# Optimization experiments

Measured on AMD Instinct MI355X. Metric: run time of the kernel, lower is better.

The kernel has to match this reference:

```python
import jax, jax.numpy as jnp
import numpy as np

# dims
V = 50000      # vocab_size
DW = 50        # word_embed_size
DP = 5         # pos_embed_size
D = DW + 2 * DP  # input_size = 60
OC = 230       # out_c
NREL = 53      # n_rel
POSV = 61      # 2*pos_limit + 1
LIMIT = 30     # piecewise split threshold
G, B, L = 1000, 8, 120  # n_bags, bag_size, sentence length


def setup_inputs() -> dict:
    key = jax.random.key(0)
    ks = jax.random.split(key, 11)
    f32 = jnp.float32
    words = jax.random.randint(ks[0], (G, B, L), 0, V, dtype=jnp.int32)
    pos = jax.random.randint(ks[1], (G, B, L, 2), 0, POSV, dtype=jnp.int32)
    # pretrained-style word embeddings + position embeddings
    w2v = jax.random.normal(ks[2], (V, DW), f32) * 0.1
    pos1_emb = jax.random.normal(ks[3], (POSV, DP), f32) * 0.1
    pos2_emb = jax.random.normal(ks[4], (POSV, DP), f32) * 0.1
    con1 = float(np.sqrt(6.0 / ((DP + DW) * 3)))
    conv_w = jax.random.uniform(ks[5], (OC, 1, 3, D), f32, -con1, con1)  # OIHW
    conv_b0 = jax.random.uniform(ks[6], (1, OC), f32, -con1, con1)
    conv_b1 = jax.random.uniform(ks[7], (1, OC), f32, -con1, con1)
    conv_b2 = jax.random.uniform(ks[8], (1, OC), f32, -con1, con1)
    con = float(np.sqrt(6.0 / (OC + NREL)))
    r_embed = jax.random.uniform(ks[9], (NREL, 3 * OC), f32, -con, con)
    r_bias = jax.random.uniform(ks[10], (NREL,), f32, -con, con)
    return dict(words=words, pos=pos, w2v=w2v, pos1_emb=pos1_emb,
                pos2_emb=pos2_emb, conv_w=conv_w, conv_b0=conv_b0,
                conv_b1=conv_b1, conv_b2=conv_b2, r_embed=r_embed,
                r_bias=r_bias)


def reference(words, pos, w2v, pos1_emb, pos2_emb, conv_w,
              conv_b0, conv_b1, conv_b2, r_embed, r_bias):
    g, bag, ln = words.shape
    n = g * bag
    w = words.reshape(n, ln)
    p = pos.reshape(n, ln, 2)
    # embedding lookups -> [N, L, D]
    x = jnp.concatenate([w2v[w], pos1_emb[p[..., 0]], pos2_emb[p[..., 1]]], axis=-1)
    # Conv1d(1, OC, (3, D), padding=(1, 0)) over [N,1,L,D] -> [N,OC,L]
    feat = jax.lax.conv_general_dilated(
        x[:, None, :, :], conv_w, window_strides=(1, 1),
        padding=((1, 1), (0, 0)),
        dimension_numbers=('NCHW', 'OIHW', 'NCHW'))[..., 0]
    # piecewise masks from position ids
    p1 = (p[..., 0] >= LIMIT).astype(feat.dtype)  # [N, L]
    p2 = (p[..., 1] >= LIMIT).astype(feat.dtype)
    left = p1 * p2
    right = (1.0 - p1) * (1.0 - p2)
    mid = 1.0 - left - right

    def pool(mask, bias):  # masked max over sequence + per-piece bias
        return jnp.max(feat * mask[:, None, :], axis=-1) + bias  # [N, OC]

    f = jnp.concatenate([pool(left, conv_b0), pool(mid, conv_b1),
                         pool(right, conv_b2)], axis=-1)  # [N, 3*OC]
    f = jnp.tanh(f)
    # eval mode: dropout identity, logits scaled by 0.5 before bias
    logits = (f @ r_embed.T) * 0.5 + r_bias  # [N, NREL]
    logp = jax.nn.log_softmax(logits, axis=-1).reshape(g, bag, NREL)
    # eval mode: max over sentences in each bag
    return jnp.max(logp, axis=1)  # [G, NREL]
```

## Files before the change

kernel.cpp:

```cpp
#include <hip/hip_runtime.h>
#include <hip/hip_bf16.h>
#include <math.h>

typedef __bf16 bf16;
typedef __bf16 bf16x4 __attribute__((ext_vector_type(4)));
typedef __bf16 bf16x8 __attribute__((ext_vector_type(8)));
typedef float f32x4 __attribute__((ext_vector_type(4)));

#define OCC 230
#define NRELS 53
#define PCAT_OFF 2500000
#define REMBB_OFF 2537216
#define CONVB_OFF 2582272
#define ZOFF 2631424
#define WS_ELEMS 2631432

union FragU { bf16x8 v8; bf16x4 v4[2]; bf16 e[8]; };

__global__ void pcnn_prep(const float* __restrict__ w2v, const float* __restrict__ p1e,
                          const float* __restrict__ p2e, const float* __restrict__ remb,
                          const float* __restrict__ convw, bf16* __restrict__ wsb) {
  const int i = blockIdx.x * 256 + threadIdx.x;
  if (i < 625000) {
    const float4 f = *reinterpret_cast<const float4*>(w2v + 4 * i);
    bf16x4 v = {(bf16)f.x, (bf16)f.y, (bf16)f.z, (bf16)f.w};
    *reinterpret_cast<bf16x4*>(wsb + 4 * i) = v;
    return;
  }
  int e = i - 625000;
  if (e < 37210) {
    const int row = e / 10, c = e - row * 10;
    const int v1 = row / 61, v2 = row - v1 * 61;
    wsb[PCAT_OFF + e] = (bf16)((c < 5) ? p1e[v1 * 5 + c] : p2e[v2 * 5 + (c - 5)]);
    return;
  }
  e -= 37210;
  if (e < 45056) {
    const int r = e / 704, c = e - r * 704;
    wsb[REMBB_OFF + e] = (r < NRELS && c < 690) ? (bf16)remb[r * 690 + c] : (bf16)0.0f;
    return;
  }
  e -= 45056;
  if (e < 49152) {
    const int oc = e / 192, k = e - oc * 192;
    wsb[CONVB_OFF + e] = (oc < OCC && k < 180) ? (bf16)convw[oc * 180 + k] : (bf16)0.0f;
    return;
  }
  e -= 49152;
  if (e < 8) wsb[ZOFF + e] = (bf16)0.0f;
}

__global__ __launch_bounds__(1024, 4)
void pcnn_bag(const int* __restrict__ words, const int* __restrict__ posi,
              const float* __restrict__ cb0, const float* __restrict__ cb1,
              const float* __restrict__ cb2, const float* __restrict__ rbias,
              const bf16* __restrict__ wsb, float* __restrict__ out)
{
  __shared__ __align__(16) bf16 xflat[2][7360];
  __shared__ __align__(16) bf16 fl_all[8][712];
  __shared__ int widx[960];
  __shared__ float poolbuf[2][3][256];
  __shared__ float logits_l[8][64];

  const int t = threadIdx.x;
  const int b = blockIdx.x;
  const int wv = t >> 6;
  const int lane = t & 63;
  const int g = lane >> 4;
  const int cl = lane & 15;
  const int mh = wv >> 3;
  const int ocp = wv & 7;

  if (t < 960) {
    const int w = words[b * 960 + t];
    const int2 pp = *reinterpret_cast<const int2*>(posi + b * 1920 + 2 * t);
    const bool b0 = pp.x >= 30, b1 = pp.y >= 30;
    const int pc = (b0 && b1) ? 0 : ((!b0 && !b1) ? 2 : 1);
    widx[t] = w | ((pp.x * 61 + pp.y) << 16) | (pc << 28);
  }
  if (t < 60) { xflat[0][t] = (bf16)0.0f; xflat[1][t] = (bf16)0.0f; }
  if (t < 112) fl_all[t / 14][690 + (t % 14)] = (bf16)0.0f;

  FragU Bf[2][6];
  {
    const bf16* cwb = wsb + CONVB_OFF;
#pragma unroll
    for (int nt = 0; nt < 2; ++nt) {
      const int oc = ocp * 32 + nt * 16 + cl;
#pragma unroll
      for (int ks = 0; ks < 6; ++ks)
        Bf[nt][ks].v8 = *reinterpret_cast<const bf16x8*>(cwb + oc * 192 + ks * 32 + g * 8);
    }
  }

  int pA = 0, ocA = 0;
  float biasA = 0.0f;
  if (t < 690) {
    pA = t / 230; ocA = t - pA * 230;
    biasA = (pA == 0 ? cb0 : pA == 1 ? cb1 : cb2)[ocA];
  }
  __syncthreads();

  auto gather_one = [&](int s, int nb, int j) {
    const int q = j * 1024 + wv * 64 + lane;
    const int qc = (q < 3600) ? q : 3599;
    const int l = qc / 30;
    const int c = qc - l * 30;
    const int wi = widx[s * 120 + l];
    const int word = wi & 0xFFFF;
    const int pidx = (wi >> 16) & 0xFFF;
    const bf16* srcd = (c < 25) ? (wsb + word * 50 + 2 * c)
                                : (wsb + PCAT_OFF + pidx * 10 + (2 * c - 50));
    const bf16* src = (q < 3600) ? srcd : (wsb + ZOFF);
    bf16* dst = &xflat[nb][60 + j * 2048 + wv * 128];
    __builtin_amdgcn_global_load_lds(
        (const __attribute__((address_space(1))) void*)src,
        (__attribute__((address_space(3))) void*)dst, 4, 0, 0);
  };
  auto issue_gather = [&](int s, int nb) {
#pragma unroll
    for (int j = 0; j < 3; ++j) gather_one(s, nb, j);
    if (wv < 9) gather_one(s, nb, 3);
  };

  issue_gather(0, 0);
  asm volatile("s_waitcnt vmcnt(0)" ::: "memory");
  __syncthreads();

  for (int s = 0; s < 8; ++s) {
    const int nb = s & 1;
    if (s < 7) issue_gather(s + 1, nb ^ 1);

    int mrow[4];
#pragma unroll
    for (int mt = 0; mt < 4; ++mt) {
      const int m = mh * 64 + mt * 16 + cl;
      mrow[mt] = (m < 120 ? m : 119) * 60;
    }

    f32x4 acc[4][2];
    const f32x4 z4 = {0.f, 0.f, 0.f, 0.f};
#pragma unroll
    for (int mt = 0; mt < 4; ++mt) { acc[mt][0] = z4; acc[mt][1] = z4; }

#pragma unroll
    for (int ks = 0; ks < 6; ++ks) {
#pragma unroll
      for (int mt = 0; mt < 4; ++mt) {
        FragU a;
        const int idx = mrow[mt] + ks * 32 + g * 8;
        a.v4[0] = *reinterpret_cast<const bf16x4*>(&xflat[nb][idx]);
        a.v4[1] = *reinterpret_cast<const bf16x4*>(&xflat[nb][idx + 4]);
#pragma unroll
        for (int nt = 0; nt < 2; ++nt)
          acc[mt][nt] = __builtin_amdgcn_mfma_f32_16x16x32_bf16(
              a.v8, Bf[nt][ks].v8, acc[mt][nt], 0, 0, 0);
      }
    }

    float pool[2][3];
#pragma unroll
    for (int nt = 0; nt < 2; ++nt) { pool[nt][0] = pool[nt][1] = pool[nt][2] = -INFINITY; }
#pragma unroll
    for (int mt = 0; mt < 4; ++mt) {
      const int l0 = mh * 64 + mt * 16 + g * 4;
      if (l0 < 120) {
        const int4 pv = *reinterpret_cast<const int4*>(&widx[s * 120 + l0]);
        const int pcs[4] = {(int)((unsigned)pv.x >> 28), (int)((unsigned)pv.y >> 28),
                            (int)((unsigned)pv.z >> 28), (int)((unsigned)pv.w >> 28)};
#pragma unroll
        for (int r = 0; r < 4; ++r) {
          const int p = pcs[r];
#pragma unroll
          for (int nt = 0; nt < 2; ++nt) {
            const float v = acc[mt][nt][r];
            pool[nt][0] = fmaxf(pool[nt][0], p == 0 ? v : 0.0f);
            pool[nt][1] = fmaxf(pool[nt][1], p == 1 ? v : 0.0f);
            pool[nt][2] = fmaxf(pool[nt][2], p == 2 ? v : 0.0f);
          }
        }
      }
    }
#pragma unroll
    for (int nt = 0; nt < 2; ++nt)
#pragma unroll
      for (int p = 0; p < 3; ++p) {
        float x = pool[nt][p];
        x = fmaxf(x, __shfl_xor(x, 16));
        x = fmaxf(x, __shfl_xor(x, 32));
        pool[nt][p] = x;
      }
    if (g == 0) {
#pragma unroll
      for (int nt = 0; nt < 2; ++nt) {
        const int oc = ocp * 32 + nt * 16 + cl;
        poolbuf[mh][0][oc] = pool[nt][0];
        poolbuf[mh][1][oc] = pool[nt][1];
        poolbuf[mh][2][oc] = pool[nt][2];
      }
    }
    __syncthreads();

    if (t < 690)
      fl_all[s][t] = (bf16)tanhf(fmaxf(poolbuf[0][pA][ocA], poolbuf[1][pA][ocA]) + biasA);

    asm volatile("s_waitcnt vmcnt(0)" ::: "memory");
    __syncthreads();
  }

  if (wv < 4) {
    f32x4 lac = {0.f, 0.f, 0.f, 0.f};
    const bf16* brow = wsb + REMBB_OFF + (wv * 16 + cl) * 704 + g * 8;
    const bf16x8 zf = {(bf16)0.f, (bf16)0.f, (bf16)0.f, (bf16)0.f,
                       (bf16)0.f, (bf16)0.f, (bf16)0.f, (bf16)0.f};
#pragma unroll
    for (int ks = 0; ks < 22; ++ks) {
      bf16x8 afr = (cl < 8)
          ? *reinterpret_cast<const bf16x8*>(&fl_all[cl][ks * 32 + g * 8]) : zf;
      const bf16x8 bfr = *reinterpret_cast<const bf16x8*>(brow + ks * 32);
      lac = __builtin_amdgcn_mfma_f32_16x16x32_bf16(afr, bfr, lac, 0, 0, 0);
    }
    if (g < 2) {
      const int rel = wv * 16 + cl;
      const float bias = (rel < NRELS) ? rbias[rel] : 0.0f;
#pragma unroll
      for (int r = 0; r < 4; ++r)
        logits_l[g * 4 + r][rel] = lac[r] * 0.5f + bias;
    }
  }
  __syncthreads();

  if (wv < 8) {
    const float x = (lane < NRELS) ? logits_l[wv][lane] : -INFINITY;
    float m = x;
#pragma unroll
    for (int off = 32; off; off >>= 1) m = fmaxf(m, __shfl_xor(m, off));
    const float e = (lane < NRELS) ? __expf(x - m) : 0.0f;
    float sm = e;
#pragma unroll
    for (int off = 32; off; off >>= 1) sm += __shfl_xor(sm, off);
    if (lane < NRELS) logits_l[wv][lane] = x - m - __logf(sm);
  }
  __syncthreads();

  if (t < NRELS) {
    float m = logits_l[0][t];
#pragma unroll
    for (int s2 = 1; s2 < 8; ++s2) m = fmaxf(m, logits_l[s2][t]);
    out[b * NRELS + t] = m;
  }
}

extern "C" void kernel_launch(void* const* d_in, const int* in_sizes, int n_in,
                              void* d_out, int out_size, void* d_ws, size_t ws_size,
                              hipStream_t stream) {
  const int* words  = (const int*)d_in[0];
  const int* posi   = (const int*)d_in[1];
  const float* w2v  = (const float*)d_in[2];
  const float* p1e  = (const float*)d_in[3];
  const float* p2e  = (const float*)d_in[4];
  const float* cw   = (const float*)d_in[5];
  const float* cb0  = (const float*)d_in[6];
  const float* cb1  = (const float*)d_in[7];
  const float* cb2  = (const float*)d_in[8];
  const float* remb = (const float*)d_in[9];
  const float* rbias= (const float*)d_in[10];
  bf16* wsb = (bf16*)d_ws;
  float* out = (float*)d_out;

  pcnn_prep<<<2955, 256, 0, stream>>>(w2v, p1e, p2e, remb, cw, wsb);
  pcnn_bag<<<1000, 1024, 0, stream>>>(words, posi, cb0, cb1, cb2, rbias, wsb, out);
}
```

Baseline: 280.7 us.

## Repack embedding and conv weights for 16-byte LDS gathers and 128-bit A loads

Splits the bf16 word table into a 48-element aligned part plus a padded tail. Pads the position-pair table to 16 elements and permutes the conv weight K dimension to match. The gather can then use 16-byte global_load_lds transfers instead of 4-byte ones, and the MFMA A-fragments become single 16-byte LDS reads from a planar layout. This cuts the number of gather instructions and LDS read ops, but adds more complex address logic and a bigger shared buffer that may hurt occupancy.

After: 297.3 us. 1.06x slower.

```diff
diff --git a/kernel.cpp b/kernel.cpp
--- a/kernel.cpp
+++ b/kernel.cpp
@@ -9,46 +9,77 @@
 
 #define OCC 230
 #define NRELS 53
-#define PCAT_OFF 2500000
-#define REMBB_OFF 2537216
-#define CONVB_OFF 2582272
-#define ZOFF 2631424
-#define WS_ELEMS 2631432
+#define W2V48_OFF 0
+#define WTAIL_OFF 2400000
+#define PCAT_OFF  2600000
+#define REMBB_OFF 2659536
+#define CONVB_OFF 2704592
+#define ZOFF      2753744
 
 union FragU { bf16x8 v8; bf16x4 v4[2]; bf16 e[8]; };
+
+__device__ __host__ inline int jmap(int j) {
+  if (j < 48) return j;
+  if (j < 53) return 50 + (j - 48);
+  if (j < 56) return 55 + (j - 53);
+  if (j < 58) return 58 + (j - 56);
+  if (j < 60) return 48 + (j - 58);
+  return -1;
+}
 
 __global__ void pcnn_prep(const float* __restrict__ w2v, const float* __restrict__ p1e,
                           const float* __restrict__ p2e, const float* __restrict__ remb,
                           const float* __restrict__ convw, bf16* __restrict__ wsb) {
   const int i = blockIdx.x * 256 + threadIdx.x;
-  if (i < 625000) {
-    const float4 f = *reinterpret_cast<const float4*>(w2v + 4 * i);
-    bf16x4 v = {(bf16)f.x, (bf16)f.y, (bf16)f.z, (bf16)f.w};
-    *reinterpret_cast<bf16x4*>(wsb + 4 * i) = v;
-    return;
-  }
-  int e = i - 625000;
-  if (e < 37210) {
-    const int row = e / 10, c = e - row * 10;
+  if (i < 300000) {
+    const int w = i / 6, c = i - 6 * w;
+    const float* s = w2v + w * 50 + c * 8;
+    bf16* d = wsb + W2V48_OFF + w * 48 + c * 8;
+#pragma unroll
+    for (int jj = 0; jj < 8; ++jj) d[jj] = (bf16)s[jj];
+    return;
+  }
+  int e = i - 300000;
+  if (e < 50000) {
+    bf16* d = wsb + WTAIL_OFF + e * 4;
+    d[0] = (bf16)w2v[e * 50 + 48];
+    d[1] = (bf16)w2v[e * 50 + 49];
+    d[2] = (bf16)0.f; d[3] = (bf16)0.f;
+    return;
+  }
+  e -= 50000;
+  if (e < 59536) {
+    const int row = e >> 4, c = e & 15;
     const int v1 = row / 61, v2 = row - v1 * 61;
-    wsb[PCAT_OFF + e] = (bf16)((c < 5) ? p1e[v1 * 5 + c] : p2e[v2 * 5 + (c - 5)]);
-    return;
-  }
-  e -= 37210;
+    float v = 0.f;
+    if (c < 5) v = p1e[v1 * 5 + c];
+    else if (c < 10) v = p2e[v2 * 5 + (c - 5)];
+    wsb[PCAT_OFF + e] = (bf16)v;
+    return;
+  }
+  e -= 59536;
   if (e < 45056) {
     const int r = e / 704, c = e - r * 704;
-    wsb[REMBB_OFF + e] = (r < NRELS && c < 690) ? (bf16)remb[r * 690 + c] : (bf16)0.0f;
+    wsb[REMBB_OFF + e] = (r < NRELS && c < 690) ? (bf16)remb[r * 690 + c] : (bf16)0.f;
     return;
   }
   e -= 45056;
   if (e < 49152) {
-    const int oc = e / 192, k = e - oc * 192;
-    wsb[CONVB_OFF + e] = (oc < OCC && k < 180) ? (bf16)convw[oc * 180 + k] : (bf16)0.0f;
+    const int oc = e / 192, kp = e - oc * 192;
+    const int tap = kp >> 6, j = kp & 63;
+    const int d = jmap(j);
+    wsb[CONVB_OFF + e] = (oc < OCC && d >= 0) ? (bf16)convw[oc * 180 + tap * 60 + d]
+                                              : (bf16)0.f;
     return;
   }
   e -= 49152;
-  if (e < 8) wsb[ZOFF + e] = (bf16)0.0f;
+  if (e < 8) wsb[ZOFF + e] = (bf16)0.f;
 }
+
+#define WPL 0
+#define TAPL 7168
+#define TBPL 8192
+#define BUFE 9216
 
 __global__ __launch_bounds__(1024, 4)
 void pcnn_bag(const int* __restrict__ words, const int* __restrict__ posi,
@@ -56,7 +87,7 @@
               const float* __restrict__ cb2, const float* __restrict__ rbias,
               const bf16* __restrict__ wsb, float* __restrict__ out)
 {
-  __shared__ __align__(16) bf16 xflat[2][7360];
+  __shared__ __align__(16) bf16 xpl[2][BUFE];
   __shared__ __align__(16) bf16 fl_all[8][712];
   __shared__ int widx[960];
   __shared__ float poolbuf[2][3][256];
@@ -78,7 +109,6 @@
     const int pc = (b0 && b1) ? 0 : ((!b0 && !b1) ? 2 : 1);
     widx[t] = w | ((pp.x * 61 + pp.y) << 16) | (pc << 28);
   }
-  if (t < 60) { xflat[0][t] = (bf16)0.0f; xflat[1][t] = (bf16)0.0f; }
   if (t < 112) fl_all[t / 14][690 + (t % 14)] = (bf16)0.0f;
 
   FragU Bf[2][6];
@@ -99,58 +129,88 @@
     pA = t / 230; ocA = t - pA * 230;
     biasA = (pA == 0 ? cb0 : pA == 1 ? cb1 : cb2)[ocA];
   }
+
+  const int wslot = wv * 64 + lane;
+  const int wlr = wslot / 7;
+  const int wc  = wslot - 7 * wlr;
+  const int taslot = (wv - 14) * 64 + lane;
+  const int tbslot = wv * 64 + lane;
+  const int tblr = tbslot >> 2;
+  const int tbp  = tbslot & 3;
+
   __syncthreads();
 
-  auto gather_one = [&](int s, int nb, int j) {
-    const int q = j * 1024 + wv * 64 + lane;
-    const int qc = (q < 3600) ? q : 3599;
-    const int l = qc / 30;
-    const int c = qc - l * 30;
-    const int wi = widx[s * 120 + l];
-    const int word = wi & 0xFFFF;
-    const int pidx = (wi >> 16) & 0xFFF;
-    const bf16* srcd = (c < 25) ? (wsb + word * 50 + 2 * c)
-                                : (wsb + PCAT_OFF + pidx * 10 + (2 * c - 50));
-    const bf16* src = (q < 3600) ? srcd : (wsb + ZOFF);
-    bf16* dst = &xflat[nb][60 + j * 2048 + wv * 128];
-    __builtin_amdgcn_global_load_lds(
-        (const __attribute__((address_space(1))) void*)src,
-        (__attribute__((address_space(3))) void*)dst, 4, 0, 0);
-  };
   auto issue_gather = [&](int s, int nb) {
-#pragma unroll
-    for (int j = 0; j < 3; ++j) gather_one(s, nb, j);
-    if (wv < 9) gather_one(s, nb, 3);
+    bf16* bufb = &xpl[nb][0];
+    const int* wrow = &widx[s * 120];
+    if (wv < 14) {
+      const bf16* src = wsb + ZOFF;
+      if (wlr >= 1 && wlr <= 120 && wc < 6) {
+        const int wi = wrow[wlr - 1];
+        src = wsb + W2V48_OFF + (wi & 0xFFFF) * 48 + wc * 8;
+      }
+      bf16* dst = bufb + WPL + wv * 512;
+      __builtin_amdgcn_global_load_lds(
+          (const __attribute__((address_space(1))) void*)src,
+          (__attribute__((address_space(3))) void*)dst, 16, 0, 0);
+    } else {
+      const bf16* src = wsb + ZOFF;
+      if (taslot >= 1 && taslot <= 120) {
+        const int wi = wrow[taslot - 1];
+        src = wsb + PCAT_OFF + (((unsigned)wi >> 16) & 0xFFF) * 16;
+      }
+      bf16* dst = bufb + TAPL + (wv - 14) * 512;
+      __builtin_amdgcn_global_load_lds(
+          (const __attribute__((address_space(1))) void*)src,
+          (__attribute__((address_space(3))) void*)dst, 16, 0, 0);
+    }
+    if (wv < 8) {
+      const bf16* src = wsb + ZOFF;
+      if (tblr >= 1 && tblr <= 120) {
+        const int wi = wrow[tblr - 1];
+        if (tbp == 0)      src = wsb + PCAT_OFF + (((unsigned)wi >> 16) & 0xFFF) * 16 + 8;
+        else if (tbp == 1) src = wsb + WTAIL_OFF + (wi & 0xFFFF) * 4;
+      }
+      bf16* dst = bufb + TBPL + wv * 128;
+      __builtin_amdgcn_global_load_lds(
+          (const __attribute__((address_space(1))) void*)src,
+          (__attribute__((address_space(3))) void*)dst, 4, 0, 0);
+    }
   };
 
   issue_gather(0, 0);
   asm volatile("s_waitcnt vmcnt(0)" ::: "memory");
   __syncthreads();
 
+  int lrb[4];
+#pragma unroll
+  for (int mt = 0; mt < 4; ++mt) {
+    const int m = mh * 64 + mt * 16 + cl;
+    lrb[mt] = (m < 120 ? m : 119);
+  }
+
   for (int s = 0; s < 8; ++s) {
     const int nb = s & 1;
     if (s < 7) issue_gather(s + 1, nb ^ 1);
 
-    int mrow[4];
-#pragma unroll
-    for (int mt = 0; mt < 4; ++mt) {
-      const int m = mh * 64 + mt * 16 + cl;
-      mrow[mt] = (m < 120 ? m : 119) * 60;
-    }
-
     f32x4 acc[4][2];
     const f32x4 z4 = {0.f, 0.f, 0.f, 0.f};
 #pragma unroll
     for (int mt = 0; mt < 4; ++mt) { acc[mt][0] = z4; acc[mt][1] = z4; }
 
+    const char* bufc = reinterpret_cast<const char*>(&xpl[nb][0]);
 #pragma unroll
     for (int ks = 0; ks < 6; ++ks) {
+      const int k0 = ks * 32 + g * 8;
+      const int tap = k0 >> 6;
+      const int j = k0 & 63;
 #pragma unroll
       for (int mt = 0; mt < 4; ++mt) {
+        const int lr = lrb[mt] + tap;
+        const int boff = (j < 48) ? (lr * 112 + j * 2)
+                                  : ((j == 48 ? (TAPL * 2) : (TBPL * 2)) + lr * 16);
         FragU a;
-        const int idx = mrow[mt] + ks * 32 + g * 8;
-        a.v4[0] = *reinterpret_cast<const bf16x4*>(&xflat[nb][idx]);
-        a.v4[1] = *reinterpret_cast<const bf16x4*>(&xflat[nb][idx + 4]);
+        a.v8 = *reinterpret_cast<const bf16x8*>(bufc + boff);
 #pragma unroll
         for (int nt = 0; nt < 2; ++nt)
           acc[mt][nt] = __builtin_amdgcn_mfma_f32_16x16x32_bf16(
@@ -268,6 +328,6 @@
   bf16* wsb = (bf16*)d_ws;
   float* out = (float*)d_out;
 
-  pcnn_prep<<<2955, 256, 0, stream>>>(w2v, p1e, p2e, remb, cw, wsb);
+  pcnn_prep<<<1968, 256, 0, stream>>>(w2v, p1e, p2e, remb, cw, wsb);
   pcnn_bag<<<1000, 1024, 0, stream>>>(words, posi, cb0, cb1, cb2, rbias, wsb, out);
 }
```

## Split fused bag kernel into per-sentence conv kernel and per-bag logits kernel

Applied to the files above, without the earlier changes.

The single 1000-block kernel, which looped over 8 sentences with a double-buffered gather, becomes two kernels. The first runs 16000 blocks of 256 threads, one per sentence and output-channel half; it writes the tanh piece features to workspace. The second runs one block per bag and does the relation matmul, log-softmax and bag max. The embedding table is re-laid out as 48-element rows plus a 2-element tail, and the position table is padded to 16, so the gather can use 16-byte loads instead of 4-byte LDS-direct loads. The aim is more parallelism and higher occupancy. In exchange, pooled features make an extra round trip through global memory and there is one more launch. The padded feature slots are never written, so the second kernel relies on them being multiplied by zero weights.

Measured after the change: 313.7 us. 1.12x slower.

```diff
diff --git a/kernel.cpp b/kernel.cpp
--- a/kernel.cpp
+++ b/kernel.cpp
@@ -9,11 +9,12 @@
 
 #define OCC 230
 #define NRELS 53
-#define PCAT_OFF 2500000
-#define REMBB_OFF 2537216
-#define CONVB_OFF 2582272
-#define ZOFF 2631424
-#define WS_ELEMS 2631432
+#define W2V48_OFF 0
+#define WTAIL_OFF 2400000
+#define PCAT_OFF  2500000
+#define REMBB_OFF 2559552
+#define CONVB_OFF 2608704
+#define FLWS_OFF  2657862
 
 union FragU { bf16x8 v8; bf16x4 v4[2]; bf16 e[8]; };
 
@@ -21,217 +22,258 @@
                           const float* __restrict__ p2e, const float* __restrict__ remb,
                           const float* __restrict__ convw, bf16* __restrict__ wsb) {
   const int i = blockIdx.x * 256 + threadIdx.x;
-  if (i < 625000) {
-    const float4 f = *reinterpret_cast<const float4*>(w2v + 4 * i);
-    bf16x4 v = {(bf16)f.x, (bf16)f.y, (bf16)f.z, (bf16)f.w};
-    *reinterpret_cast<bf16x4*>(wsb + 4 * i) = v;
+  if (i < 300000) {
+    const int w = i / 6, c = i - 6 * w;
+    const float2* s = reinterpret_cast<const float2*>(w2v + w * 50 + c * 8);
+    const float2 f0 = s[0], f1 = s[1], f2 = s[2], f3 = s[3];
+    bf16x8 v = {(bf16)f0.x, (bf16)f0.y, (bf16)f1.x, (bf16)f1.y,
+                (bf16)f2.x, (bf16)f2.y, (bf16)f3.x, (bf16)f3.y};
+    *reinterpret_cast<bf16x8*>(wsb + W2V48_OFF + w * 48 + c * 8) = v;
     return;
   }
-  int e = i - 625000;
-  if (e < 37210) {
-    const int row = e / 10, c = e - row * 10;
+  int e = i - 300000;
+  if (e < 50000) {
+    const float2 f = *reinterpret_cast<const float2*>(w2v + e * 50 + 48);
+    wsb[WTAIL_OFF + 2 * e]     = (bf16)f.x;
+    wsb[WTAIL_OFF + 2 * e + 1] = (bf16)f.y;
+    return;
+  }
+  e -= 50000;
+  if (e < 7442) {
+    const int row = e >> 1, h = e & 1;
     const int v1 = row / 61, v2 = row - v1 * 61;
-    wsb[PCAT_OFF + e] = (bf16)((c < 5) ? p1e[v1 * 5 + c] : p2e[v2 * 5 + (c - 5)]);
+    bf16x8 v;
+    if (h == 0) {
+      v[0] = (bf16)p1e[v1 * 5 + 0]; v[1] = (bf16)p1e[v1 * 5 + 1];
+      v[2] = (bf16)p1e[v1 * 5 + 2]; v[3] = (bf16)p1e[v1 * 5 + 3];
+      v[4] = (bf16)p1e[v1 * 5 + 4]; v[5] = (bf16)p2e[v2 * 5 + 0];
+      v[6] = (bf16)0.f; v[7] = (bf16)0.f;
+    } else {
+      v[0] = (bf16)p2e[v2 * 5 + 1]; v[1] = (bf16)p2e[v2 * 5 + 2];
+      v[2] = (bf16)p2e[v2 * 5 + 3]; v[3] = (bf16)p2e[v2 * 5 + 4];
+      v[4] = (bf16)0.f; v[5] = (bf16)0.f; v[6] = (bf16)0.f; v[7] = (bf16)0.f;
+    }
+    *reinterpret_cast<bf16x8*>(wsb + PCAT_OFF + row * 16 + h * 8) = v;
     return;
   }
-  e -= 37210;
-  if (e < 45056) {
-    const int r = e / 704, c = e - r * 704;
-    wsb[REMBB_OFF + e] = (r < NRELS && c < 690) ? (bf16)remb[r * 690 + c] : (bf16)0.0f;
+  e -= 7442;
+  if (e < 6144) {
+    const int r = e / 96, c0 = (e - r * 96) * 8;
+    bf16x8 v;
+#pragma unroll
+    for (int j = 0; j < 8; ++j) {
+      const int cc = c0 + j, p = cc >> 8, oc = cc & 255;
+      v[j] = (r < NRELS && oc < OCC) ? (bf16)remb[r * 690 + p * OCC + oc] : (bf16)0.f;
+    }
+    *reinterpret_cast<bf16x8*>(wsb + REMBB_OFF + r * 768 + c0) = v;
     return;
   }
-  e -= 45056;
-  if (e < 49152) {
-    const int oc = e / 192, k = e - oc * 192;
-    wsb[CONVB_OFF + e] = (oc < OCC && k < 180) ? (bf16)convw[oc * 180 + k] : (bf16)0.0f;
-    return;
-  }
-  e -= 49152;
-  if (e < 8) wsb[ZOFF + e] = (bf16)0.0f;
+  e -= 6144;
+  if (e < 6144) {
+    const int oc = e / 24, k0 = (e - oc * 24) * 8;
+    bf16x8 v;
+#pragma unroll
+    for (int j = 0; j < 8; ++j) {
+      const int k = k0 + j;
+      v[j] = (oc < OCC && k < 180) ? (bf16)convw[oc * 180 + k] : (bf16)0.f;
+    }
+    *reinterpret_cast<bf16x8*>(wsb + CONVB_OFF + oc * 192 + k0) = v;
+  }
 }
 
-__global__ __launch_bounds__(1024, 4)
-void pcnn_bag(const int* __restrict__ words, const int* __restrict__ posi,
-              const float* __restrict__ cb0, const float* __restrict__ cb1,
-              const float* __restrict__ cb2, const float* __restrict__ rbias,
-              const bf16* __restrict__ wsb, float* __restrict__ out)
+#define XE 7352
+
+__global__ __launch_bounds__(256, 3)
+void pcnn_conv(const int* __restrict__ words, const int* __restrict__ posi,
+               const float* __restrict__ cb0, const float* __restrict__ cb1,
+               const float* __restrict__ cb2, const bf16* __restrict__ wsb,
+               bf16* __restrict__ flws)
 {
-  __shared__ __align__(16) bf16 xflat[2][7360];
-  __shared__ __align__(16) bf16 fl_all[8][712];
-  __shared__ int widx[960];
-  __shared__ float poolbuf[2][3][256];
-  __shared__ float logits_l[8][64];
+  __shared__ __align__(16) bf16 xlds[XE];
+  __shared__ int widx[120];
 
   const int t = threadIdx.x;
-  const int b = blockIdx.x;
-  const int wv = t >> 6;
-  const int lane = t & 63;
-  const int g = lane >> 4;
-  const int cl = lane & 15;
-  const int mh = wv >> 3;
-  const int ocp = wv & 7;
-
-  if (t < 960) {
-    const int w = words[b * 960 + t];
-    const int2 pp = *reinterpret_cast<const int2*>(posi + b * 1920 + 2 * t);
+  const int bid = blockIdx.x;
+  const int ns = bid >> 1;
+  const int ochalf = bid & 1;
+  const int wv = t >> 6, lane = t & 63, g = lane >> 4, cl = lane & 15;
+
+  if (t < 120) {
+    const int w = words[ns * 120 + t];
+    const int2 pp = *reinterpret_cast<const int2*>(posi + ns * 240 + 2 * t);
     const bool b0 = pp.x >= 30, b1 = pp.y >= 30;
     const int pc = (b0 && b1) ? 0 : ((!b0 && !b1) ? 2 : 1);
     widx[t] = w | ((pp.x * 61 + pp.y) << 16) | (pc << 28);
   }
-  if (t < 60) { xflat[0][t] = (bf16)0.0f; xflat[1][t] = (bf16)0.0f; }
-  if (t < 112) fl_all[t / 14][690 + (t % 14)] = (bf16)0.0f;
+  if (t < 16) {
+    const int r = (t >> 3) ? 121 : 0;
+    const int gr = t & 7;
+    const int eo = r * 60 + ((gr < 7) ? gr * 8 : 52);
+    *reinterpret_cast<int2*>(&xlds[eo])     = int2{0, 0};
+    *reinterpret_cast<int2*>(&xlds[eo + 4]) = int2{0, 0};
+  }
 
   FragU Bf[2][6];
   {
     const bf16* cwb = wsb + CONVB_OFF;
 #pragma unroll
     for (int nt = 0; nt < 2; ++nt) {
-      const int oc = ocp * 32 + nt * 16 + cl;
+      const int oc = ochalf * 128 + wv * 32 + nt * 16 + cl;
 #pragma unroll
       for (int ks = 0; ks < 6; ++ks)
         Bf[nt][ks].v8 = *reinterpret_cast<const bf16x8*>(cwb + oc * 192 + ks * 32 + g * 8);
     }
   }
-
-  int pA = 0, ocA = 0;
-  float biasA = 0.0f;
-  if (t < 690) {
-    pA = t / 230; ocA = t - pA * 230;
-    biasA = (pA == 0 ? cb0 : pA == 1 ? cb1 : cb2)[ocA];
-  }
-  __syncthreads();
-
-  auto gather_one = [&](int s, int nb, int j) {
-    const int q = j * 1024 + wv * 64 + lane;
-    const int qc = (q < 3600) ? q : 3599;
-    const int l = qc / 30;
-    const int c = qc - l * 30;
-    const int wi = widx[s * 120 + l];
-    const int word = wi & 0xFFFF;
-    const int pidx = (wi >> 16) & 0xFFF;
-    const bf16* srcd = (c < 25) ? (wsb + word * 50 + 2 * c)
-                                : (wsb + PCAT_OFF + pidx * 10 + (2 * c - 50));
-    const bf16* src = (q < 3600) ? srcd : (wsb + ZOFF);
-    bf16* dst = &xflat[nb][60 + j * 2048 + wv * 128];
+  __syncthreads();
+
+#pragma unroll
+  for (int k = 0; k < 4; ++k) {
+    const int gi = t + k * 256;
+    if (gi < 960) {
+      const int lr = 1 + (gi >> 3), gr = gi & 7;
+      const int wi = widx[lr - 1];
+      const int word = wi & 0xFFFF;
+      const int pidx = (wi >> 16) & 0xFFF;
+      if (gr < 6) {
+        const int4 v = *reinterpret_cast<const int4*>(wsb + W2V48_OFF + word * 48 + gr * 8);
+        bf16* d = &xlds[lr * 60 + gr * 8];
+        *reinterpret_cast<int2*>(d)     = int2{v.x, v.y};
+        *reinterpret_cast<int2*>(d + 4) = int2{v.z, v.w};
+      } else if (gr == 6) {
+        const int wt = *(reinterpret_cast<const int*>(wsb + WTAIL_OFF) + word);
+        const int4 pc4 = *reinterpret_cast<const int4*>(wsb + PCAT_OFF + pidx * 16);
+        bf16* d = &xlds[lr * 60 + 48];
+        *reinterpret_cast<int2*>(d)     = int2{wt, pc4.x};
+        *reinterpret_cast<int2*>(d + 4) = int2{pc4.y, pc4.z};
+      } else {
+        const int2 v = *reinterpret_cast<const int2*>(wsb + PCAT_OFF + pidx * 16 + 8);
+        *reinterpret_cast<int2*>(&xlds[lr * 60 + 56]) = v;
+      }
+    }
+  }
+  __syncthreads();
+
+  int mrow[8];
+#pragma unroll
+  for (int mt = 0; mt < 8; ++mt) {
+    const int m = mt * 16 + cl;
+    mrow[mt] = (m < 120 ? m : 119) * 60;
+  }
+
+  f32x4 acc[8][2];
+  const f32x4 z4 = {0.f, 0.f, 0.f, 0.f};
+#pragma unroll
+  for (int mt = 0; mt < 8; ++mt) { acc[mt][0] = z4; acc[mt][1] = z4; }
+
+#pragma unroll
+  for (int ks = 0; ks < 6; ++ks) {
+    const int ko = ks * 32 + g * 8;
+#pragma unroll
+    for (int mt = 0; mt < 8; ++mt) {
+      FragU a;
+      a.v4[0] = *reinterpret_cast<const bf16x4*>(&xlds[mrow[mt] + ko]);
+      a.v4[1] = *reinterpret_cast<const bf16x4*>(&xlds[mrow[mt] + ko + 4]);
+#pragma unroll
+      for (int nt = 0; nt < 2; ++nt)
+        acc[mt][nt] = __builtin_amdgcn_mfma_f32_16x16x32_bf16(
+            a.v8, Bf[nt][ks].v8, acc[mt][nt], 0, 0, 0);
+    }
+  }
+
+  float pool[2][3];
+#pragma unroll
+  for (int nt = 0; nt < 2; ++nt) { pool[nt][0] = pool[nt][1] = pool[nt][2] = -INFINITY; }
+#pragma unroll
+  for (int mt = 0; mt < 8; ++mt) {
+    const int l0 = mt * 16 + g * 4;
+    if (l0 < 120) {
+      const int4 pv = *reinterpret_cast<const int4*>(&widx[l0]);
+      const int pcs[4] = {(int)((unsigned)pv.x >> 28), (int)((unsigned)pv.y >> 28),
+                          (int)((unsigned)pv.z >> 28), (int)((unsigned)pv.w >> 28)};
+#pragma unroll
+      for (int r = 0; r < 4; ++r) {
+        const int p = pcs[r];
+#pragma unroll
+        for (int nt = 0; nt < 2; ++nt) {
+          const float v = acc[mt][nt][r];
+          pool[nt][0] = fmaxf(pool[nt][0], p == 0 ? v : 0.0f);
+          pool[nt][1] = fmaxf(pool[nt][1], p == 1 ? v : 0.0f);
+          pool[nt][2] = fmaxf(pool[nt][2], p == 2 ? v : 0.0f);
+        }
+      }
+    }
+  }
+#pragma unroll
+  for (int nt = 0; nt < 2; ++nt)
+#pragma unroll
+    for (int p = 0; p < 3; ++p) {
+      float x = pool[nt][p];
+      x = fmaxf(x, __shfl_xor(x, 16));
+      x = fmaxf(x, __shfl_xor(x, 32));
+      pool[nt][p] = x;
+    }
+
+  if (g == 0) {
+#pragma unroll
+    for (int nt = 0; nt < 2; ++nt) {
+      const int ocg = ochalf * 128 + wv * 32 + nt * 16 + cl;
+      if (ocg < OCC) {
+        const float b0v = cb0[ocg], b1v = cb1[ocg], b2v = cb2[ocg];
+        bf16* fr = flws + ns * 768;
+        fr[ocg]       = (bf16)tanhf(pool[nt][0] + b0v);
+        fr[256 + ocg] = (bf16)tanhf(pool[nt][1] + b1v);
+        fr[512 + ocg] = (bf16)tanhf(pool[nt][2] + b2v);
+      }
+    }
+  }
+}
+
+__global__ __launch_bounds__(256)
+void pcnn_logits(const bf16* __restrict__ wsb, const bf16* __restrict__ flws,
+                 const float* __restrict__ rbias, float* __restrict__ out)
+{
+  __shared__ __align__(16) bf16 fl_lds[6144];
+  __shared__ float logits_l[8][64];
+
+  const int t = threadIdx.x;
+  const int bag = blockIdx.x;
+  const int wv = t >> 6, lane = t & 63, g = lane >> 4, cl = lane & 15;
+
+#pragma unroll
+  for (int j = 0; j < 3; ++j) {
+    const bf16* src = flws + bag * 6144 + (j * 256 + t) * 8;
+    bf16* dst = &fl_lds[(j * 256 + wv * 64) * 8];
     __builtin_amdgcn_global_load_lds(
         (const __attribute__((address_space(1))) void*)src,
-        (__attribute__((address_space(3))) void*)dst, 4, 0, 0);
-  };
-  auto issue_gather = [&](int s, int nb) {
-#pragma unroll
-    for (int j = 0; j < 3; ++j) gather_one(s, nb, j);
-    if (wv < 9) gather_one(s, nb, 3);
-  };
-
-  issue_gather(0, 0);
+        (__attribute__((address_space(3))) void*)dst, 16, 0, 0);
+  }
   asm volatile("s_waitcnt vmcnt(0)" ::: "memory");
   __syncthreads();
 
-  for (int s = 0; s < 8; ++s) {
-    const int nb = s & 1;
-    if (s < 7) issue_gather(s + 1, nb ^ 1);
-
-    int mrow[4];
-#pragma unroll
-    for (int mt = 0; mt < 4; ++mt) {
-      const int m = mh * 64 + mt * 16 + cl;
-      mrow[mt] = (m < 120 ? m : 119) * 60;
-    }
-
-    f32x4 acc[4][2];
-    const f32x4 z4 = {0.f, 0.f, 0.f, 0.f};
-#pragma unroll
-    for (int mt = 0; mt < 4; ++mt) { acc[mt][0] = z4; acc[mt][1] = z4; }
-
-#pragma unroll
-    for (int ks = 0; ks < 6; ++ks) {
-#pragma unroll
-      for (int mt = 0; mt < 4; ++mt) {
-        FragU a;
-        const int idx = mrow[mt] + ks * 32 + g * 8;
-        a.v4[0] = *reinterpret_cast<const bf16x4*>(&xflat[nb][idx]);
-        a.v4[1] = *reinterpret_cast<const bf16x4*>(&xflat[nb][idx + 4]);
-#pragma unroll
-        for (int nt = 0; nt < 2; ++nt)
-          acc[mt][nt] = __builtin_amdgcn_mfma_f32_16x16x32_bf16(
-              a.v8, Bf[nt][ks].v8, acc[mt][nt], 0, 0, 0);
-      }
-    }
-
-    float pool[2][3];
-#pragma unroll
-    for (int nt = 0; nt < 2; ++nt) { pool[nt][0] = pool[nt][1] = pool[nt][2] = -INFINITY; }
-#pragma unroll
-    for (int mt = 0; mt < 4; ++mt) {
-      const int l0 = mh * 64 + mt * 16 + g * 4;
-      if (l0 < 120) {
-        const int4 pv = *reinterpret_cast<const int4*>(&widx[s * 120 + l0]);
-        const int pcs[4] = {(int)((unsigned)pv.x >> 28), (int)((unsigned)pv.y >> 28),
-                            (int)((unsigned)pv.z >> 28), (int)((unsigned)pv.w >> 28)};
-#pragma unroll
-        for (int r = 0; r < 4; ++r) {
-          const int p = pcs[r];
-#pragma unroll
-          for (int nt = 0; nt < 2; ++nt) {
-            const float v = acc[mt][nt][r];
-            pool[nt][0] = fmaxf(pool[nt][0], p == 0 ? v : 0.0f);
-            pool[nt][1] = fmaxf(pool[nt][1], p == 1 ? v : 0.0f);
-            pool[nt][2] = fmaxf(pool[nt][2], p == 2 ? v : 0.0f);
-          }
-        }
-      }
-    }
-#pragma unroll
-    for (int nt = 0; nt < 2; ++nt)
-#pragma unroll
-      for (int p = 0; p < 3; ++p) {
-        float x = pool[nt][p];
-        x = fmaxf(x, __shfl_xor(x, 16));
-        x = fmaxf(x, __shfl_xor(x, 32));
-        pool[nt][p] = x;
-      }
-    if (g == 0) {
-#pragma unroll
-      for (int nt = 0; nt < 2; ++nt) {
-        const int oc = ocp * 32 + nt * 16 + cl;
-        poolbuf[mh][0][oc] = pool[nt][0];
-        poolbuf[mh][1][oc] = pool[nt][1];
-        poolbuf[mh][2][oc] = pool[nt][2];
-      }
-    }
-    __syncthreads();
-
-    if (t < 690)
-      fl_all[s][t] = (bf16)tanhf(fmaxf(poolbuf[0][pA][ocA], poolbuf[1][pA][ocA]) + biasA);
-
-    asm volatile("s_waitcnt vmcnt(0)" ::: "memory");
-    __syncthreads();
-  }
-
-  if (wv < 4) {
-    f32x4 lac = {0.f, 0.f, 0.f, 0.f};
-    const bf16* brow = wsb + REMBB_OFF + (wv * 16 + cl) * 704 + g * 8;
-    const bf16x8 zf = {(bf16)0.f, (bf16)0.f, (bf16)0.f, (bf16)0.f,
-                       (bf16)0.f, (bf16)0.f, (bf16)0.f, (bf16)0.f};
-#pragma unroll
-    for (int ks = 0; ks < 22; ++ks) {
-      bf16x8 afr = (cl < 8)
-          ? *reinterpret_cast<const bf16x8*>(&fl_all[cl][ks * 32 + g * 8]) : zf;
-      const bf16x8 bfr = *reinterpret_cast<const bf16x8*>(brow + ks * 32);
-      lac = __builtin_amdgcn_mfma_f32_16x16x32_bf16(afr, bfr, lac, 0, 0, 0);
-    }
-    if (g < 2) {
-      const int rel = wv * 16 + cl;
-      const float bias = (rel < NRELS) ? rbias[rel] : 0.0f;
-#pragma unroll
-      for (int r = 0; r < 4; ++r)
-        logits_l[g * 4 + r][rel] = lac[r] * 0.5f + bias;
-    }
-  }
-  __syncthreads();
-
-  if (wv < 8) {
-    const float x = (lane < NRELS) ? logits_l[wv][lane] : -INFINITY;
+  f32x4 lac = {0.f, 0.f, 0.f, 0.f};
+  const bf16* brow = wsb + REMBB_OFF + (wv * 16 + cl) * 768 + g * 8;
+  const bf16x8 zf = {(bf16)0.f, (bf16)0.f, (bf16)0.f, (bf16)0.f,
+                     (bf16)0.f, (bf16)0.f, (bf16)0.f, (bf16)0.f};
+#pragma unroll
+  for (int ks = 0; ks < 24; ++ks) {
+    const bf16x8 afr = (cl < 8)
+        ? *reinterpret_cast<const bf16x8*>(&fl_lds[cl * 768 + ks * 32 + g * 8]) : zf;
+    const bf16x8 bfr = *reinterpret_cast<const bf16x8*>(brow + ks * 32);
+    lac = __builtin_amdgcn_mfma_f32_16x16x32_bf16(afr, bfr, lac, 0, 0, 0);
+  }
+  if (g < 2) {
+    const int rel = wv * 16 + cl;
+    const float bias = (rel < NRELS) ? rbias[rel] : 0.0f;
+#pragma unroll
+    for (int r = 0; r < 4; ++r)
+      logits_l[g * 4 + r][rel] = lac[r] * 0.5f + bias;
+  }
+  __syncthreads();
+
+#pragma unroll
+  for (int rep = 0; rep < 2; ++rep) {
+    const int s = wv + rep * 4;
+    const float x = (lane < NRELS) ? logits_l[s][lane] : -INFINITY;
     float m = x;
 #pragma unroll
     for (int off = 32; off; off >>= 1) m = fmaxf(m, __shfl_xor(m, off));
@@ -239,7 +281,7 @@
     float sm = e;
 #pragma unroll
     for (int off = 32; off; off >>= 1) sm += __shfl_xor(sm, off);
-    if (lane < NRELS) logits_l[wv][lane] = x - m - __logf(sm);
+    if (lane < NRELS) logits_l[s][lane] = x - m - __logf(sm);
   }
   __syncthreads();
 
@@ -247,7 +289,7 @@
     float m = logits_l[0][t];
 #pragma unroll
     for (int s2 = 1; s2 < 8; ++s2) m = fmaxf(m, logits_l[s2][t]);
-    out[b * NRELS + t] = m;
+    out[bag * NRELS + t] = m;
   }
 }
 
@@ -266,8 +308,10 @@
   const float* remb = (const float*)d_in[9];
   const float* rbias= (const float*)d_in[10];
   bf16* wsb = (bf16*)d_ws;
+  bf16* flws = wsb + FLWS_OFF;
   float* out = (float*)d_out;
 
-  pcnn_prep<<<2955, 256, 0, stream>>>(w2v, p1e, p2e, remb, cw, wsb);
-  pcnn_bag<<<1000, 1024, 0, stream>>>(words, posi, cb0, cb1, cb2, rbias, wsb, out);
+  pcnn_prep<<<1445, 256, 0, stream>>>(w2v, p1e, p2e, remb, cw, wsb);
+  pcnn_conv<<<16000, 256, 0, stream>>>(words, posi, cb0, cb1, cb2, wsb, flws);
+  pcnn_logits<<<1000, 256, 0, stream>>>(wsb, flws, rbias, out);
 }
```
